# Kernel optimization log

Measured on AMD Instinct MI355X. Metric: run time of the kernel, lower is better.

Reference implementation:

```python
import jax, jax.numpy as jnp
import numpy as np

B, N, M, DQ, DK, DV, H = 8, 1024, 1024, 512, 512, 512, 8
DS = DV // H  # dim_split = 64
NEG = -1e38


def _ln(x, g, b, eps=1e-5):
    mu = jnp.mean(x, -1, keepdims=True)
    var = jnp.mean((x - mu) ** 2, -1, keepdims=True)
    return (x - mu) * jax.lax.rsqrt(var + eps) * g + b


def setup_inputs() -> dict:
    key = jax.random.key(0)
    ks = jax.random.split(key, 16)
    s = 0.02
    return {
        "x": jax.random.normal(ks[0], (B, N, DQ), jnp.float32),
        "y": jax.random.normal(ks[1], (B, M, DK), jnp.float32),
        "x_mask": jax.random.randint(ks[2], (B, N), 0, 2).astype(bool),
        "y_mask": jax.random.randint(ks[3], (B, M), 0, 2).astype(bool),
        "Wq": jax.random.normal(ks[4], (DQ, DV), jnp.float32) * s,
        "Wk": jax.random.normal(ks[5], (DK, DV), jnp.float32) * s,
        "Wv": jax.random.normal(ks[6], (DK, DV), jnp.float32) * s,
        "Wo": jax.random.normal(ks[7], (DV, DQ), jnp.float32) * s,
        "W1": jax.random.normal(ks[8], (DQ, DQ), jnp.float32) * s,
        "b1": jnp.zeros((DQ,), jnp.float32),
        "W2": jax.random.normal(ks[9], (DQ, DQ), jnp.float32) * s,
        "b2": jnp.zeros((DQ,), jnp.float32),
        "g1": jnp.ones((DQ,), jnp.float32),
        "be1": jnp.zeros((DQ,), jnp.float32),
        "g2": jnp.ones((DQ,), jnp.float32),
        "be2": jnp.zeros((DQ,), jnp.float32),
    }


def reference(x, y, x_mask, y_mask, Wq, Wk, Wv, Wo, W1, b1, W2, b2, g1, be1, g2, be2):
    xm = x_mask[..., None]  # [B,N,1]
    ym = y_mask[..., None]  # [B,M,1]
    x = jnp.where(xm, 0.0, x)
    y = jnp.where(ym, 0.0, y)
    # projections (no bias); masked rows stay zero, re-mask as in source
    q = jnp.where(xm, 0.0, x @ Wq).reshape(B, N, H, DS)
    k = jnp.where(ym, 0.0, y @ Wk).reshape(B, M, H, DS)
    v = jnp.where(ym, 0.0, y @ Wv).reshape(B, M, H, DS)
    # scaled dot product; NOTE: scale is sqrt(dim_v), faithful to source
    sdp = jnp.einsum('bnhd,bmhd->bhnm', q, k) / np.sqrt(DV)
    mask = x_mask[:, None, :, None] | y_mask[:, None, None, :]  # [B,1,N,M]
    sdp = jnp.where(mask, NEG, sdp)
    alpha = jax.nn.softmax(sdp, axis=-1)  # softmax over keys (slot_att=False)
    att = jnp.einsum('bhnm,bmhd->bnhd', alpha, v).reshape(B, N, DV)
    att = jnp.where(xm, 0.0, att)
    o = x + att @ Wo
    o = _ln(o, g1, be1)
    ff = jax.nn.relu(o @ W1 + b1) @ W2 + b2
    o = _ln(o + ff, g2, be2)
    return jnp.where(xm, 0.0, o)
```

## Files before the change

### kernel.cpp

```cpp
#include <hip/hip_runtime.h>
#include <hip/hip_bf16.h>

typedef __bf16 bf16;
typedef __attribute__((ext_vector_type(4))) __bf16 bf16x4;
typedef __attribute__((ext_vector_type(8))) __bf16 bf16x8;
typedef __attribute__((ext_vector_type(4))) float f32x4;

#define B_ 8
#define N_ 1024
#define M_ 1024
#define H_ 8
#define ROWS_ (B_ * N_)

__device__ __forceinline__ f32x4 mfma16(bf16x8 a, bf16x8 b, f32x4 c) {
    return __builtin_amdgcn_mfma_f32_16x16x32_bf16(a, b, c, 0, 0, 0);
}

__device__ __forceinline__ void glds16(const void* g, void* l) {
    __builtin_amdgcn_global_load_lds((const __attribute__((address_space(1))) void*)g,
                                     (__attribute__((address_space(3))) void*)l, 16, 0, 0);
}

__global__ __launch_bounds__(256) void prep(const float* __restrict__ x, const float* __restrict__ y,
                                            bf16* __restrict__ Xb, bf16* __restrict__ Yb,
                                            const float* W0, const float* W1, const float* W2,
                                            const float* W3, const float* W4, const float* W5,
                                            bf16* T0, bf16* T1, bf16* T2, bf16* T3, bf16* T4, bf16* T5) {
    __shared__ float t[64][65];
    int bid = blockIdx.x;
    if (bid < 8192) {
        int i = bid * 256 + threadIdx.x;
        const float4* s;
        bf16x4* d;
        int j;
        if (i < 1048576) { s = (const float4*)x; d = (bf16x4*)Xb; j = i; }
        else             { s = (const float4*)y; d = (bf16x4*)Yb; j = i - 1048576; }
        float4 f = s[j];
        bf16x4 o = {(bf16)f.x, (bf16)f.y, (bf16)f.z, (bf16)f.w};
        d[j] = o;
        return;
    }
    int wb = bid - 8192;
    const float* srcs[6] = {W0, W1, W2, W3, W4, W5};
    bf16* dsts[6] = {T0, T1, T2, T3, T4, T5};
    const float* W = srcs[wb >> 6];
    bf16* Wt = dsts[wb >> 6];
    int tile = wb & 63;
    int k0 = (tile >> 3) * 64, n0 = (tile & 7) * 64;
    int tx = threadIdx.x & 63, ty = threadIdx.x >> 6;
#pragma unroll
    for (int j = 0; j < 16; ++j)
        t[ty + j * 4][tx] = W[(size_t)(k0 + ty + j * 4) * 512 + n0 + tx];
    __syncthreads();
#pragma unroll
    for (int j = 0; j < 16; ++j)
        Wt[(size_t)(n0 + ty + j * 4) * 512 + k0 + tx] = (bf16)t[tx][ty + j * 4];
}

__device__ __forceinline__ void gemm_core(const bf16* __restrict__ A, const bf16* __restrict__ Bt,
                                          int row0, int col0, char* AsB, char* BsB, f32x4 acc[2][4]) {
    int tid = threadIdx.x, wave = tid >> 6, lane = tid & 63;
    int lr = lane & 15, q4 = lane >> 4;
    const bf16 *Asrc[4], *Bsrc[2];
#pragma unroll
    for (int s = 0; s < 4; ++s) {
        int c = tid + s * 256, r = c >> 3, bk = (c & 7) ^ (r & 7);
        Asrc[s] = A + (size_t)(row0 + r) * 512 + bk * 8;
    }
#pragma unroll
    for (int s = 0; s < 2; ++s) {
        int c = tid + s * 256, r = c >> 3, bk = (c & 7) ^ (r & 7);
        Bsrc[s] = Bt + (size_t)(col0 + r) * 512 + bk * 8;
    }
    int wb = wave * 1024;
#pragma unroll
    for (int s = 0; s < 4; ++s) glds16(Asrc[s], AsB + s * 4096 + wb);
#pragma unroll
    for (int s = 0; s < 2; ++s) glds16(Bsrc[s], BsB + s * 4096 + wb);
#pragma unroll
    for (int it = 0; it < 8; ++it) {
        __syncthreads();
        const char* Ac = AsB + (it & 1) * 16384;
        const char* Bc = BsB + (it & 1) * 8192;
        if (it < 7) {
            char* An = AsB + ((it + 1) & 1) * 16384;
            char* Bn = BsB + ((it + 1) & 1) * 8192;
            int k0 = (it + 1) * 64;
#pragma unroll
            for (int s = 0; s < 4; ++s) glds16(Asrc[s] + k0, An + s * 4096 + wb);
#pragma unroll
            for (int s = 0; s < 2; ++s) glds16(Bsrc[s] + k0, Bn + s * 4096 + wb);
        }
        bf16x8 af[2][2], bfr[4][2];
#pragma unroll
        for (int rt = 0; rt < 2; ++rt) {
            int row = wave * 32 + rt * 16 + lr;
#pragma unroll
            for (int c = 0; c < 2; ++c)
                af[rt][c] = *(const bf16x8*)(Ac + (row * 8 + ((c * 4 + q4) ^ (row & 7))) * 16);
        }
#pragma unroll
        for (int ct = 0; ct < 4; ++ct) {
            int col = ct * 16 + lr;
#pragma unroll
            for (int c = 0; c < 2; ++c)
                bfr[ct][c] = *(const bf16x8*)(Bc + (col * 8 + ((c * 4 + q4) ^ (col & 7))) * 16);
        }
#pragma unroll
        for (int rt = 0; rt < 2; ++rt)
#pragma unroll
            for (int ct = 0; ct < 4; ++ct) {
                acc[rt][ct] = mfma16(af[rt][0], bfr[ct][0], acc[rt][ct]);
                acc[rt][ct] = mfma16(af[rt][1], bfr[ct][1], acc[rt][ct]);
            }
    }
}

__global__ __launch_bounds__(256, 2) void proj_qkv(const bf16* __restrict__ Xb, const bf16* __restrict__ Yb,
                                                   const bf16* __restrict__ Wqt, const bf16* __restrict__ Wkt,
                                                   const bf16* __restrict__ Wvt,
                                                   bf16* __restrict__ qb, bf16* __restrict__ kb,
                                                   bf16* __restrict__ Vt) {
    __shared__ char AsB[2 * 16384];
    __shared__ char BsB[2 * 8192];
    int z = blockIdx.z;
    const bf16 *A, *Bt;
    int row0, col0;
    if (z == 0)      { A = Xb;  Bt = Wqt; row0 = blockIdx.x * 128; col0 = blockIdx.y * 64; }
    else if (z == 1) { A = Yb;  Bt = Wkt; row0 = blockIdx.x * 128; col0 = blockIdx.y * 64; }
    else { A = Wvt; Bt = Yb; int flat = blockIdx.y * 64 + blockIdx.x; row0 = (flat & 3) * 128; col0 = (flat >> 2) * 64; }
    const f32x4 z4 = {0.f, 0.f, 0.f, 0.f};
    f32x4 acc[2][4] = {{z4, z4, z4, z4}, {z4, z4, z4, z4}};
    gemm_core(A, Bt, row0, col0, AsB, BsB, acc);
    int wave = threadIdx.x >> 6, lane = threadIdx.x & 63, lr = lane & 15, q4 = lane >> 4;
    bf16* dst = (z == 0) ? qb : kb;
#pragma unroll
    for (int rt = 0; rt < 2; ++rt)
#pragma unroll
        for (int ct = 0; ct < 4; ++ct) {
            int col = col0 + ct * 16 + lr;
#pragma unroll
            for (int r = 0; r < 4; ++r) {
                int row = row0 + wave * 32 + rt * 16 + q4 * 4 + r;
                bf16 v = (bf16)acc[rt][ct][r];
                if (z < 2) dst[(size_t)row * 512 + col] = v;
                else Vt[(size_t)((col >> 10) * 512 + row) * 1024 + (col & 1023)] = v;
            }
        }
}

template <int MODE>
__global__ __launch_bounds__(256, 2) void gemm_bt(const bf16* __restrict__ A, const bf16* __restrict__ Bt,
                                                  const float* __restrict__ bias, void* __restrict__ Cout) {
    __shared__ char AsB[2 * 16384];
    __shared__ char BsB[2 * 8192];
    int row0 = blockIdx.x * 128, col0 = blockIdx.y * 64;
    const f32x4 z4 = {0.f, 0.f, 0.f, 0.f};
    f32x4 acc[2][4] = {{z4, z4, z4, z4}, {z4, z4, z4, z4}};
    gemm_core(A, Bt, row0, col0, AsB, BsB, acc);
    int wave = threadIdx.x >> 6, lane = threadIdx.x & 63, lr = lane & 15, q4 = lane >> 4;
#pragma unroll
    for (int rt = 0; rt < 2; ++rt)
#pragma unroll
        for (int ct = 0; ct < 4; ++ct) {
            int col = col0 + ct * 16 + lr;
            float bv = (MODE >= 2) ? bias[col] : 0.0f;
#pragma unroll
            for (int r = 0; r < 4; ++r) {
                int row = row0 + wave * 32 + rt * 16 + q4 * 4 + r;
                float v = acc[rt][ct][r] + bv;
                if (MODE == 3) v = fmaxf(v, 0.0f);
                if (MODE == 3) ((bf16*)Cout)[(size_t)row * 512 + col] = (bf16)v;
                else           ((float*)Cout)[(size_t)row * 512 + col] = v;
            }
        }
}

__global__ __launch_bounds__(256, 2) void attn(const bf16* __restrict__ Q, const bf16* __restrict__ Kb,
                                               const bf16* __restrict__ Vt, const int* __restrict__ ymask,
                                               bf16* __restrict__ att) {
    __shared__ bf16 Ks[2][64 * 64];
    __shared__ bf16 Vs[2][64 * 64];
    __shared__ bf16 Ps[4][32 * 72];

    int bid = blockIdx.x;
    int bh = bid & 63, n0 = (bid >> 6) * 128;
    int b = bh >> 3, h = bh & 7;
    int tid = threadIdx.x, wave = tid >> 6, lane = tid & 63;
    int lr = lane & 15, q4 = lane >> 4;
    const float scale = 0.044194173824159216f;

    bf16x8 aq[2][2];
#pragma unroll
    for (int rt = 0; rt < 2; ++rt) {
        const bf16* qp = Q + (size_t)((b << 10) + n0 + wave * 32 + rt * 16 + lr) * 512 + h * 64 + q4 * 8;
        aq[rt][0] = *(const bf16x8*)qp;
        aq[rt][1] = *(const bf16x8*)(qp + 32);
    }

    const bf16 *Ksrc[2], *Vsrc[2];
#pragma unroll
    for (int s = 0; s < 2; ++s) {
        int c = tid + s * 256, r = c >> 3, bk = (c & 7) ^ (r & 7);
        Ksrc[s] = Kb + (size_t)((b << 10) + r) * 512 + h * 64 + bk * 8;
        Vsrc[s] = Vt + (size_t)(b * 512 + h * 64 + r) * 1024 + bk * 8;
    }
    int wb = wave * 1024;
    const int* ymb = ymask + (b << 10);

    const f32x4 zv = {0.f, 0.f, 0.f, 0.f};
    f32x4 O[2][4];
    float lsum[2][4];
#pragma unroll
    for (int rt = 0; rt < 2; ++rt) {
#pragma unroll
        for (int dt = 0; dt < 4; ++dt) O[rt][dt] = zv;
#pragma unroll
        for (int rr = 0; rr < 4; ++rr) lsum[rt][rr] = 0.f;
    }

#pragma unroll
    for (int s = 0; s < 2; ++s) {
        glds16(Ksrc[s], (char*)Ks[0] + s * 4096 + wb);
        glds16(Vsrc[s], (char*)Vs[0] + s * 4096 + wb);
    }

    for (int it = 0; it < 16; ++it) {
        __syncthreads();
        const char* K_ = (const char*)Ks[it & 1];
        const char* V_ = (const char*)Vs[it & 1];
        if (it < 15) {
            char* Kn = (char*)Ks[(it + 1) & 1];
            char* Vn = (char*)Vs[(it + 1) & 1];
            size_t m1 = (size_t)(it + 1) * 64;
#pragma unroll
            for (int s = 0; s < 2; ++s) {
                glds16(Ksrc[s] + m1 * 512, Kn + s * 4096 + wb);
                glds16(Vsrc[s] + m1, Vn + s * 4096 + wb);
            }
        }
        int m0 = it * 64;

#pragma unroll
        for (int nt = 0; nt < 4; ++nt) {
            int krow = nt * 16 + lr;
            bf16x8 kf0 = *(const bf16x8*)(K_ + (krow * 8 + (q4 ^ (krow & 7))) * 16);
            bf16x8 kf1 = *(const bf16x8*)(K_ + (krow * 8 + ((4 + q4) ^ (krow & 7))) * 16);
            float fm = ymb[m0 + krow] ? -1e30f : 0.0f;
#pragma unroll
            for (int rt = 0; rt < 2; ++rt) {
                f32x4 s = mfma16(aq[rt][0], kf0, zv);
                s = mfma16(aq[rt][1], kf1, s);
#pragma unroll
                for (int rr = 0; rr < 4; ++rr) {
                    float p = __expf(fmaf(s[rr], scale, fm));
                    lsum[rt][rr] += p;
                    Ps[wave][(rt * 16 + q4 * 4 + rr) * 72 + krow] = (bf16)p;
                }
            }
        }
        bf16x8 ap[2][2];
#pragma unroll
        for (int rt = 0; rt < 2; ++rt) {
            ap[rt][0] = *(const bf16x8*)&Ps[wave][(rt * 16 + lr) * 72 + q4 * 8];
            ap[rt][1] = *(const bf16x8*)&Ps[wave][(rt * 16 + lr) * 72 + 32 + q4 * 8];
        }
#pragma unroll
        for (int dt = 0; dt < 4; ++dt) {
            int vrow = dt * 16 + lr;
            bf16x8 vf0 = *(const bf16x8*)(V_ + (vrow * 8 + (q4 ^ (vrow & 7))) * 16);
            bf16x8 vf1 = *(const bf16x8*)(V_ + (vrow * 8 + ((4 + q4) ^ (vrow & 7))) * 16);
#pragma unroll
            for (int rt = 0; rt < 2; ++rt) {
                O[rt][dt] = mfma16(ap[rt][0], vf0, O[rt][dt]);
                O[rt][dt] = mfma16(ap[rt][1], vf1, O[rt][dt]);
            }
        }
    }

#pragma unroll
    for (int rt = 0; rt < 2; ++rt)
#pragma unroll
        for (int rr = 0; rr < 4; ++rr) {
            float v = lsum[rt][rr];
            v += __shfl_xor(v, 1); v += __shfl_xor(v, 2);
            v += __shfl_xor(v, 4); v += __shfl_xor(v, 8);
            lsum[rt][rr] = (v > 0.0f) ? (1.0f / v) : 0.0f;
        }
#pragma unroll
    for (int rt = 0; rt < 2; ++rt)
#pragma unroll
        for (int dt = 0; dt < 4; ++dt)
#pragma unroll
            for (int rr = 0; rr < 4; ++rr) {
                int row = n0 + wave * 32 + rt * 16 + q4 * 4 + rr;
                att[(size_t)((b << 10) + row) * 512 + h * 64 + dt * 16 + lr] =
                    (bf16)(O[rt][dt][rr] * lsum[rt][rr]);
            }
}

__global__ __launch_bounds__(128) void ln1_k(const float* __restrict__ X, const float* __restrict__ R,
                                             const float* __restrict__ g, const float* __restrict__ be,
                                             float* __restrict__ O, bf16* __restrict__ Obf) {
    int row = blockIdx.x, t = threadIdx.x;
    float4 xv = ((const float4*)(X + (size_t)row * 512))[t];
    float4 rv = ((const float4*)(R + (size_t)row * 512))[t];
    float4 o = {xv.x + rv.x, xv.y + rv.y, xv.z + rv.z, xv.w + rv.w};
    float s = o.x + o.y + o.z + o.w;
    float sq = o.x * o.x + o.y * o.y + o.z * o.z + o.w * o.w;
#pragma unroll
    for (int off = 1; off < 64; off <<= 1) { s += __shfl_xor(s, off); sq += __shfl_xor(sq, off); }
    __shared__ float ls[2], lq[2];
    if ((t & 63) == 0) { ls[t >> 6] = s; lq[t >> 6] = sq; }
    __syncthreads();
    s = ls[0] + ls[1]; sq = lq[0] + lq[1];
    float mu = s * (1.0f / 512.0f);
    float var = sq * (1.0f / 512.0f) - mu * mu;
    float rs = rsqrtf(var + 1e-5f);
    float4 gv = ((const float4*)g)[t];
    float4 bv = ((const float4*)be)[t];
    float4 r4 = {(o.x - mu) * rs * gv.x + bv.x, (o.y - mu) * rs * gv.y + bv.y,
                 (o.z - mu) * rs * gv.z + bv.z, (o.w - mu) * rs * gv.w + bv.w};
    ((float4*)(O + (size_t)row * 512))[t] = r4;
    bf16x4 b4 = {(bf16)r4.x, (bf16)r4.y, (bf16)r4.z, (bf16)r4.w};
    ((bf16x4*)(Obf + (size_t)row * 512))[t] = b4;
}

__global__ __launch_bounds__(128) void ln2_k(const float* __restrict__ O, const float* __restrict__ F,
                                             const float* __restrict__ g, const float* __restrict__ be,
                                             const int* __restrict__ xmask, float* __restrict__ out) {
    int row = blockIdx.x, t = threadIdx.x;
    float4 xv = ((const float4*)(O + (size_t)row * 512))[t];
    float4 rv = ((const float4*)(F + (size_t)row * 512))[t];
    float4 o = {xv.x + rv.x, xv.y + rv.y, xv.z + rv.z, xv.w + rv.w};
    float s = o.x + o.y + o.z + o.w;
    float sq = o.x * o.x + o.y * o.y + o.z * o.z + o.w * o.w;
#pragma unroll
    for (int off = 1; off < 64; off <<= 1) { s += __shfl_xor(s, off); sq += __shfl_xor(sq, off); }
    __shared__ float ls[2], lq[2];
    if ((t & 63) == 0) { ls[t >> 6] = s; lq[t >> 6] = sq; }
    __syncthreads();
    s = ls[0] + ls[1]; sq = lq[0] + lq[1];
    float mu = s * (1.0f / 512.0f);
    float var = sq * (1.0f / 512.0f) - mu * mu;
    float rs = rsqrtf(var + 1e-5f);
    int msk = xmask[row];
    float4 gv = ((const float4*)g)[t];
    float4 bv = ((const float4*)be)[t];
    float4 r4 = {(o.x - mu) * rs * gv.x + bv.x, (o.y - mu) * rs * gv.y + bv.y,
                 (o.z - mu) * rs * gv.z + bv.z, (o.w - mu) * rs * gv.w + bv.w};
    if (msk) r4 = {0.f, 0.f, 0.f, 0.f};
    ((float4*)(out + (size_t)row * 512))[t] = r4;
}

extern "C" void kernel_launch(void* const* d_in, const int* in_sizes, int n_in,
                              void* d_out, int out_size, void* d_ws, size_t ws_size,
                              hipStream_t stream) {
    const float* x   = (const float*)d_in[0];
    const float* y   = (const float*)d_in[1];
    const int*   xm  = (const int*)d_in[2];
    const int*   ym  = (const int*)d_in[3];
    const float* Wq  = (const float*)d_in[4];
    const float* Wk  = (const float*)d_in[5];
    const float* Wv  = (const float*)d_in[6];
    const float* Wo  = (const float*)d_in[7];
    const float* W1  = (const float*)d_in[8];
    const float* b1  = (const float*)d_in[9];
    const float* W2  = (const float*)d_in[10];
    const float* b2  = (const float*)d_in[11];
    const float* g1  = (const float*)d_in[12];
    const float* be1 = (const float*)d_in[13];
    const float* g2  = (const float*)d_in[14];
    const float* be2 = (const float*)d_in[15];

    char* ws = (char*)d_ws;
    const size_t WT_SZ  = 512 * 512 * sizeof(bf16);
    const size_t XB_SZ  = (size_t)ROWS_ * 512 * sizeof(bf16);
    const size_t F32_SZ = (size_t)ROWS_ * 512 * sizeof(float);

    bf16* Wqt = (bf16*)(ws + 0 * WT_SZ);
    bf16* Wkt = (bf16*)(ws + 1 * WT_SZ);
    bf16* Wvt = (bf16*)(ws + 2 * WT_SZ);
    bf16* Wot = (bf16*)(ws + 3 * WT_SZ);
    bf16* W1t = (bf16*)(ws + 4 * WT_SZ);
    bf16* W2t = (bf16*)(ws + 5 * WT_SZ);
    size_t off = 6 * WT_SZ;
    bf16* Xb  = (bf16*)(ws + off); off += XB_SZ;
    bf16* Yb  = (bf16*)(ws + off); off += XB_SZ;
    bf16* qb  = (bf16*)(ws + off); off += XB_SZ;
    bf16* kb  = (bf16*)(ws + off); off += XB_SZ;
    bf16* Vt  = (bf16*)(ws + off); off += XB_SZ;
    float* awo = (float*)(ws + off); off += F32_SZ;
    float* ob  = (float*)(ws + off); off += F32_SZ;
    bf16* attb = Xb;
    bf16* obf  = qb;
    bf16* hb   = Yb;
    float* fb  = awo;

    prep<<<8576, 256, 0, stream>>>(x, y, Xb, Yb, Wq, Wk, Wv, Wo, W1, W2,
                                   Wqt, Wkt, Wvt, Wot, W1t, W2t);

    proj_qkv<<<dim3(64, 8, 3), 256, 0, stream>>>(Xb, Yb, Wqt, Wkt, Wvt, qb, kb, Vt);

    attn<<<512, 256, 0, stream>>>(qb, kb, Vt, ym, attb);

    dim3 gg(64, 8);
    gemm_bt<0><<<gg, 256, 0, stream>>>(attb, Wot, nullptr, awo);
    ln1_k<<<ROWS_, 128, 0, stream>>>(x, awo, g1, be1, ob, obf);
    gemm_bt<3><<<gg, 256, 0, stream>>>(obf, W1t, b1, hb);
    gemm_bt<2><<<gg, 256, 0, stream>>>(hb, W2t, b2, fb);
    ln2_k<<<ROWS_, 128, 0, stream>>>(ob, fb, g2, be2, xm, (float*)d_out);
}
```

Before: 219.6 us.

## Shrink attention tile to 64 queries, single-buffer K/V, raise occupancy

The attention kernel now gives each block 64 query rows, one 16-row tile per wave, and launches twice as many blocks. K/V double buffering is dropped in favour of a single LDS buffer loaded between two barriers. The y-mask is precomputed into LDS as an additive bias that seeds the MFMA accumulator, and softmax uses exp2f with the scale folded in. The aim is higher occupancy (launch bounds 4) and less per-iteration ALU work. The cost is that K/V is reloaded twice as often overall and load latency is no longer hidden by prefetch within a block.

```diff
diff --git a/kernel.cpp b/kernel.cpp
--- a/kernel.cpp
+++ b/kernel.cpp
@@ -176,27 +176,31 @@
         }
 }
 
-__global__ __launch_bounds__(256, 2) void attn(const bf16* __restrict__ Q, const bf16* __restrict__ Kb,
+__global__ __launch_bounds__(256, 4) void attn(const bf16* __restrict__ Q, const bf16* __restrict__ Kb,
                                                const bf16* __restrict__ Vt, const int* __restrict__ ymask,
                                                bf16* __restrict__ att) {
-    __shared__ bf16 Ks[2][64 * 64];
-    __shared__ bf16 Vs[2][64 * 64];
-    __shared__ bf16 Ps[4][32 * 72];
+    __shared__ bf16 Ks[64 * 64];
+    __shared__ bf16 Vs[64 * 64];
+    __shared__ bf16 Ps[4][16 * 72];
+    __shared__ float fmk[1024];
 
     int bid = blockIdx.x;
-    int bh = bid & 63, n0 = (bid >> 6) * 128;
+    int bh = bid & 63, n0 = (bid >> 6) * 64;
     int b = bh >> 3, h = bh & 7;
     int tid = threadIdx.x, wave = tid >> 6, lane = tid & 63;
     int lr = lane & 15, q4 = lane >> 4;
-    const float scale = 0.044194173824159216f;
-
-    bf16x8 aq[2][2];
-#pragma unroll
-    for (int rt = 0; rt < 2; ++rt) {
-        const bf16* qp = Q + (size_t)((b << 10) + n0 + wave * 32 + rt * 16 + lr) * 512 + h * 64 + q4 * 8;
-        aq[rt][0] = *(const bf16x8*)qp;
-        aq[rt][1] = *(const bf16x8*)(qp + 32);
-    }
+    const float cl = 0.06376373228f;
+
+    const int* ymb = ymask + (b << 10);
+#pragma unroll
+    for (int j = 0; j < 4; ++j) {
+        int i = tid + j * 256;
+        fmk[i] = ymb[i] ? -1e38f : 0.0f;
+    }
+
+    const bf16* qp = Q + (size_t)((b << 10) + n0 + wave * 16 + lr) * 512 + h * 64 + q4 * 8;
+    bf16x8 aq0 = *(const bf16x8*)qp;
+    bf16x8 aq1 = *(const bf16x8*)(qp + 32);
 
     const bf16 *Ksrc[2], *Vsrc[2];
 #pragma unroll
@@ -206,97 +210,64 @@
         Vsrc[s] = Vt + (size_t)(b * 512 + h * 64 + r) * 1024 + bk * 8;
     }
     int wb = wave * 1024;
-    const int* ymb = ymask + (b << 10);
 
     const f32x4 zv = {0.f, 0.f, 0.f, 0.f};
-    f32x4 O[2][4];
-    float lsum[2][4];
-#pragma unroll
-    for (int rt = 0; rt < 2; ++rt) {
-#pragma unroll
-        for (int dt = 0; dt < 4; ++dt) O[rt][dt] = zv;
-#pragma unroll
-        for (int rr = 0; rr < 4; ++rr) lsum[rt][rr] = 0.f;
-    }
-
-#pragma unroll
-    for (int s = 0; s < 2; ++s) {
-        glds16(Ksrc[s], (char*)Ks[0] + s * 4096 + wb);
-        glds16(Vsrc[s], (char*)Vs[0] + s * 4096 + wb);
-    }
+    f32x4 O[4] = {zv, zv, zv, zv};
+    float lsum[4] = {0.f, 0.f, 0.f, 0.f};
 
     for (int it = 0; it < 16; ++it) {
         __syncthreads();
-        const char* K_ = (const char*)Ks[it & 1];
-        const char* V_ = (const char*)Vs[it & 1];
-        if (it < 15) {
-            char* Kn = (char*)Ks[(it + 1) & 1];
-            char* Vn = (char*)Vs[(it + 1) & 1];
-            size_t m1 = (size_t)(it + 1) * 64;
-#pragma unroll
-            for (int s = 0; s < 2; ++s) {
-                glds16(Ksrc[s] + m1 * 512, Kn + s * 4096 + wb);
-                glds16(Vsrc[s] + m1, Vn + s * 4096 + wb);
-            }
-        }
-        int m0 = it * 64;
+        size_t m0 = (size_t)it * 64;
+#pragma unroll
+        for (int s = 0; s < 2; ++s) {
+            glds16(Ksrc[s] + m0 * 512, (char*)Ks + s * 4096 + wb);
+            glds16(Vsrc[s] + m0, (char*)Vs + s * 4096 + wb);
+        }
+        __syncthreads();
 
 #pragma unroll
         for (int nt = 0; nt < 4; ++nt) {
             int krow = nt * 16 + lr;
-            bf16x8 kf0 = *(const bf16x8*)(K_ + (krow * 8 + (q4 ^ (krow & 7))) * 16);
-            bf16x8 kf1 = *(const bf16x8*)(K_ + (krow * 8 + ((4 + q4) ^ (krow & 7))) * 16);
-            float fm = ymb[m0 + krow] ? -1e30f : 0.0f;
-#pragma unroll
-            for (int rt = 0; rt < 2; ++rt) {
-                f32x4 s = mfma16(aq[rt][0], kf0, zv);
-                s = mfma16(aq[rt][1], kf1, s);
-#pragma unroll
-                for (int rr = 0; rr < 4; ++rr) {
-                    float p = __expf(fmaf(s[rr], scale, fm));
-                    lsum[rt][rr] += p;
-                    Ps[wave][(rt * 16 + q4 * 4 + rr) * 72 + krow] = (bf16)p;
-                }
+            bf16x8 kf0 = *(const bf16x8*)((const char*)Ks + (krow * 8 + (q4 ^ (krow & 7))) * 16);
+            bf16x8 kf1 = *(const bf16x8*)((const char*)Ks + (krow * 8 + ((4 + q4) ^ (krow & 7))) * 16);
+            float fm = fmk[it * 64 + krow];
+            f32x4 s = {fm, fm, fm, fm};
+            s = mfma16(aq0, kf0, s);
+            s = mfma16(aq1, kf1, s);
+#pragma unroll
+            for (int rr = 0; rr < 4; ++rr) {
+                float p = exp2f(s[rr] * cl);
+                lsum[rr] += p;
+                Ps[wave][(q4 * 4 + rr) * 72 + krow] = (bf16)p;
             }
         }
-        bf16x8 ap[2][2];
-#pragma unroll
-        for (int rt = 0; rt < 2; ++rt) {
-            ap[rt][0] = *(const bf16x8*)&Ps[wave][(rt * 16 + lr) * 72 + q4 * 8];
-            ap[rt][1] = *(const bf16x8*)&Ps[wave][(rt * 16 + lr) * 72 + 32 + q4 * 8];
-        }
+        bf16x8 ap0 = *(const bf16x8*)&Ps[wave][lr * 72 + q4 * 8];
+        bf16x8 ap1 = *(const bf16x8*)&Ps[wave][lr * 72 + 32 + q4 * 8];
 #pragma unroll
         for (int dt = 0; dt < 4; ++dt) {
             int vrow = dt * 16 + lr;
-            bf16x8 vf0 = *(const bf16x8*)(V_ + (vrow * 8 + (q4 ^ (vrow & 7))) * 16);
-            bf16x8 vf1 = *(const bf16x8*)(V_ + (vrow * 8 + ((4 + q4) ^ (vrow & 7))) * 16);
-#pragma unroll
-            for (int rt = 0; rt < 2; ++rt) {
-                O[rt][dt] = mfma16(ap[rt][0], vf0, O[rt][dt]);
-                O[rt][dt] = mfma16(ap[rt][1], vf1, O[rt][dt]);
-            }
-        }
-    }
-
-#pragma unroll
-    for (int rt = 0; rt < 2; ++rt)
+            bf16x8 vf0 = *(const bf16x8*)((const char*)Vs + (vrow * 8 + (q4 ^ (vrow & 7))) * 16);
+            bf16x8 vf1 = *(const bf16x8*)((const char*)Vs + (vrow * 8 + ((4 + q4) ^ (vrow & 7))) * 16);
+            O[dt] = mfma16(ap0, vf0, O[dt]);
+            O[dt] = mfma16(ap1, vf1, O[dt]);
+        }
+    }
+
+#pragma unroll
+    for (int rr = 0; rr < 4; ++rr) {
+        float v = lsum[rr];
+        v += __shfl_xor(v, 1); v += __shfl_xor(v, 2);
+        v += __shfl_xor(v, 4); v += __shfl_xor(v, 8);
+        lsum[rr] = (v > 0.0f) ? (1.0f / v) : 0.0f;
+    }
+#pragma unroll
+    for (int dt = 0; dt < 4; ++dt)
 #pragma unroll
         for (int rr = 0; rr < 4; ++rr) {
-            float v = lsum[rt][rr];
-            v += __shfl_xor(v, 1); v += __shfl_xor(v, 2);
-            v += __shfl_xor(v, 4); v += __shfl_xor(v, 8);
-            lsum[rt][rr] = (v > 0.0f) ? (1.0f / v) : 0.0f;
-        }
-#pragma unroll
-    for (int rt = 0; rt < 2; ++rt)
-#pragma unroll
-        for (int dt = 0; dt < 4; ++dt)
-#pragma unroll
-            for (int rr = 0; rr < 4; ++rr) {
-                int row = n0 + wave * 32 + rt * 16 + q4 * 4 + rr;
-                att[(size_t)((b << 10) + row) * 512 + h * 64 + dt * 16 + lr] =
-                    (bf16)(O[rt][dt][rr] * lsum[rt][rr]);
-            }
+            int row = n0 + wave * 16 + q4 * 4 + rr;
+            att[(size_t)((b << 10) + row) * 512 + h * 64 + dt * 16 + lr] =
+                (bf16)(O[dt][rr] * lsum[rr]);
+        }
 }
 
 __global__ __launch_bounds__(128) void ln1_k(const float* __restrict__ X, const float* __restrict__ R,
@@ -402,7 +373,7 @@
 
     proj_qkv<<<dim3(64, 8, 3), 256, 0, stream>>>(Xb, Yb, Wqt, Wkt, Wvt, qb, kb, Vt);
 
-    attn<<<512, 256, 0, stream>>>(qb, kb, Vt, ym, attb);
+    attn<<<1024, 256, 0, stream>>>(qb, kb, Vt, ym, attb);
 
     dim3 gg(64, 8);
     gemm_bt<0><<<gg, 256, 0, stream>>>(attb, Wot, nullptr, awo);
```

After: 226.2 us. 3.0% more time.
